# Kernel optimization log

Hardware: AMD Instinct MI355X
Metric: run time of the kernel (lower is better)

Reference implementation:

```python
import jax, jax.numpy as jnp
import numpy as np

ALPHA = 1.0
N, P, D = 8192, 128, 256
NUM_CLASSES = 128


def setup_inputs() -> dict:
    key = jax.random.key(0)
    kx, ky, kp = jax.random.split(key, 3)
    x = jax.random.normal(kx, (N, D), dtype=jnp.float32)
    y = jax.random.randint(ky, (N,), 0, NUM_CLASSES)
    prototypes = jax.random.normal(kp, (P, D), dtype=jnp.float32)
    return {"x": x, "y": y, "prototypes": prototypes}


def reference(x, y, prototypes):
    # (same math as the broadcasted sum((x-p)**2), expressed as a GEMM)
    x_sq = jnp.sum(x * x, axis=1, keepdims=True)          # [N, 1]
    p_sq = jnp.sum(prototypes * prototypes, axis=1)       # [P]
    dist = x_sq - 2.0 * jnp.einsum('nd,pd->np', x, prototypes) + p_sq[None, :]  # [N, P]

    # Torch code sets correct_mask[arange(N), y] = True, i.e. the "correct"
    # prototype is the one whose INDEX equals the class label y.
    n_idx = jnp.arange(dist.shape[0])
    d1 = dist[n_idx, y]                                    # [N] distance to correct prototype
    incorrect = jnp.where(jax.nn.one_hot(y, dist.shape[1], dtype=jnp.bool_),
                          jnp.inf, dist)
    d2 = jnp.min(incorrect, axis=1)                        # [N] min over wrong prototypes

    mu = (d1 - d2) / (d1 + d2)
    return jnp.mean(jax.nn.sigmoid(-ALPHA * mu))
```

## Files before the change

kernel.cpp:

```cpp
#include <hip/hip_runtime.h>
#include <math.h>

#define N_ROWS  8192
#define DIM     256
#define NPROTO  128
#define ROWS_PB 16
#define NBLK    (N_ROWS / ROWS_PB)
#define PSTR    264

typedef float f32x4 __attribute__((ext_vector_type(4)));
typedef short s16x8 __attribute__((ext_vector_type(8)));

__device__ __forceinline__ unsigned short f2bf(float f) {
  unsigned int u = __float_as_uint(f);
  u += 0x7fffu + ((u >> 16) & 1u);
  return (unsigned short)(u >> 16);
}

__global__ __launch_bounds__(256, 2) void glvq_kernel(
    const float* __restrict__ x, const int* __restrict__ y,
    const float* __restrict__ proto, float* __restrict__ out) {
  __shared__ unsigned short pT[NPROTO * PSTR];
  __shared__ unsigned short xT[ROWS_PB * PSTR];
  __shared__ float psq[NPROTO];
  __shared__ float xsq[ROWS_PB];
  __shared__ int   ylds[ROWS_PB];
  __shared__ float red1[4 * ROWS_PB];
  __shared__ float red2[4 * ROWS_PB];

  const int t = threadIdx.x;
  const int r0 = blockIdx.x * ROWS_PB;

  {
    const float4* p4 = (const float4*)proto;
#pragma unroll
    for (int j = 0; j < 16; ++j) {
      int c = j * 256 + t;
      float4 a = p4[c * 2];
      float4 b = p4[c * 2 + 1];
      int p = c >> 5;
      int ci = c & 31;
      union { s16x8 v; unsigned short u[8]; } pk;
      pk.u[0] = f2bf(a.x); pk.u[1] = f2bf(a.y); pk.u[2] = f2bf(a.z); pk.u[3] = f2bf(a.w);
      pk.u[4] = f2bf(b.x); pk.u[5] = f2bf(b.y); pk.u[6] = f2bf(b.z); pk.u[7] = f2bf(b.w);
      *(s16x8*)&pT[p * PSTR + ci * 8] = pk.v;
      float s = a.x * a.x + a.y * a.y + a.z * a.z + a.w * a.w +
                b.x * b.x + b.y * b.y + b.z * b.z + b.w * b.w;
#pragma unroll
      for (int m = 1; m <= 16; m <<= 1) s += __shfl_xor(s, m);
      if ((t & 31) == 0) psq[j * 8 + (t >> 5)] = s;
    }
  }

  {
    const float4* x4 = (const float4*)x;
    int r = t >> 4, ci = t & 15;
    const float4* xr = x4 + (size_t)(r0 + r) * (DIM / 4);
    float s = 0.f;
#pragma unroll
    for (int j = 0; j < 4; ++j) {
      float4 v = xr[ci + 16 * j];
      s += v.x * v.x + v.y * v.y + v.z * v.z + v.w * v.w;
      uint2 w2;
      w2.x = (unsigned)f2bf(v.x) | ((unsigned)f2bf(v.y) << 16);
      w2.y = (unsigned)f2bf(v.z) | ((unsigned)f2bf(v.w) << 16);
      *(uint2*)&xT[r * PSTR + (ci + 16 * j) * 4] = w2;
    }
#pragma unroll
    for (int m = 1; m <= 8; m <<= 1) s += __shfl_xor(s, m);
    if (ci == 0) xsq[r] = s;
    if (t < ROWS_PB) ylds[t] = y[r0 + t];
  }
  __syncthreads();

  const int l = t & 63;
  const int w = t >> 6;
  const int mq = l >> 4;
  const int mc = l & 15;
  f32x4 acc0 = {0.f, 0.f, 0.f, 0.f};
  f32x4 acc1 = {0.f, 0.f, 0.f, 0.f};
  const unsigned short* aptr = &xT[mc * PSTR + mq * 8];
  const unsigned short* b0p  = &pT[(w * 32 + mc) * PSTR + mq * 8];
  const unsigned short* b1p  = b0p + 16 * PSTR;
#pragma unroll
  for (int ks = 0; ks < 8; ++ks) {
    s16x8 af  = *(const s16x8*)(aptr + ks * 32);
    s16x8 bf0 = *(const s16x8*)(b0p + ks * 32);
    s16x8 bf1 = *(const s16x8*)(b1p + ks * 32);
    acc0 = __builtin_amdgcn_mfma_f32_16x16x32_bf16(af, bf0, acc0, 0, 0, 0);
    acc1 = __builtin_amdgcn_mfma_f32_16x16x32_bf16(af, bf1, acc1, 0, 0, 0);
  }

  const int p0i = w * 32 + mc;
  const int p1i = p0i + 16;
  const float pq0 = psq[p0i];
  const float pq1 = psq[p1i];
  float r1[4], r2[4];
#pragma unroll
  for (int reg = 0; reg < 4; ++reg) {
    int m = mq * 4 + reg;
    float xs = xsq[m];
    int ym = ylds[m];
    float d0 = xs + pq0 - 2.f * acc0[reg];
    float d1_ = xs + pq1 - 2.f * acc1[reg];
    float dd1 = 1e30f, dd2 = 1e30f;
    if (p0i == ym) dd1 = d0; else dd2 = d0;
    if (p1i == ym) dd1 = fminf(dd1, d1_); else dd2 = fminf(dd2, d1_);
    r1[reg] = dd1;
    r2[reg] = dd2;
  }
#pragma unroll
  for (int m = 1; m <= 8; m <<= 1) {
#pragma unroll
    for (int reg = 0; reg < 4; ++reg) {
      r1[reg] = fminf(r1[reg], __shfl_xor(r1[reg], m));
      r2[reg] = fminf(r2[reg], __shfl_xor(r2[reg], m));
    }
  }
  if (mc == 0) {
#pragma unroll
    for (int reg = 0; reg < 4; ++reg) {
      red1[w * ROWS_PB + mq * 4 + reg] = r1[reg];
      red2[w * ROWS_PB + mq * 4 + reg] = r2[reg];
    }
  }
  __syncthreads();

  if (t < ROWS_PB) {
    float d1 = 1e30f, d2 = 1e30f;
#pragma unroll
    for (int wv = 0; wv < 4; ++wv) {
      d1 = fminf(d1, red1[wv * ROWS_PB + t]);
      d2 = fminf(d2, red2[wv * ROWS_PB + t]);
    }
    float mu = (d1 - d2) / (d1 + d2);
    float s = 1.f / (1.f + __expf(mu));
#pragma unroll
    for (int m = 1; m <= 8; m <<= 1) s += __shfl_xor(s, m);
    if (t == 0) atomicAdd(out, s * (1.f / (float)N_ROWS));
  }
}

extern "C" void kernel_launch(void* const* d_in, const int* in_sizes, int n_in,
                              void* d_out, int out_size, void* d_ws, size_t ws_size,
                              hipStream_t stream) {
  const float* x = (const float*)d_in[0];
  const int* y = (const int*)d_in[1];
  const float* proto = (const float*)d_in[2];
  float* out = (float*)d_out;

  hipMemsetAsync(out, 0, sizeof(float), stream);
  glvq_kernel<<<NBLK, 256, 0, stream>>>(x, y, proto, out);
}
```

Before: 75.94 us.

## Precompute bf16 prototypes and norms in a prep kernel shared by all blocks

Adds a small prep kernel that converts the prototypes to bf16 once, computes their squared norms and zeroes the output, replacing the memset. The main kernel then loads the prebuilt bf16 prototypes straight into LDS, halving the per-block prototype read and removing the per-block conversion and shuffle reductions. The cost is an extra kernel launch with a dependency on it, plus workspace traffic.

```diff
diff --git a/kernel.cpp b/kernel.cpp
--- a/kernel.cpp
+++ b/kernel.cpp
@@ -17,9 +17,26 @@
   return (unsigned short)(u >> 16);
 }
 
+__global__ __launch_bounds__(256) void glvq_prep_kernel(
+    const float* __restrict__ proto, unsigned short* __restrict__ pbf,
+    float* __restrict__ psq, float* __restrict__ out) {
+  const int tid = blockIdx.x * 256 + threadIdx.x;
+  float4 v = ((const float4*)proto)[tid];
+  uint2 w2;
+  w2.x = (unsigned)f2bf(v.x) | ((unsigned)f2bf(v.y) << 16);
+  w2.y = (unsigned)f2bf(v.z) | ((unsigned)f2bf(v.w) << 16);
+  *(uint2*)&pbf[tid * 4] = w2;
+  float s = v.x * v.x + v.y * v.y + v.z * v.z + v.w * v.w;
+#pragma unroll
+  for (int m = 1; m <= 32; m <<= 1) s += __shfl_xor(s, m);
+  if ((threadIdx.x & 63) == 0) psq[tid >> 6] = s;
+  if (tid == 0) out[0] = 0.f;
+}
+
 __global__ __launch_bounds__(256, 2) void glvq_kernel(
     const float* __restrict__ x, const int* __restrict__ y,
-    const float* __restrict__ proto, float* __restrict__ out) {
+    const unsigned short* __restrict__ pbf, const float* __restrict__ psq_g,
+    float* __restrict__ out) {
   __shared__ unsigned short pT[NPROTO * PSTR];
   __shared__ unsigned short xT[ROWS_PB * PSTR];
   __shared__ float psq[NPROTO];
@@ -32,24 +49,16 @@
   const int r0 = blockIdx.x * ROWS_PB;
 
   {
-    const float4* p4 = (const float4*)proto;
+    const uint4* src = (const uint4*)pbf;
 #pragma unroll
     for (int j = 0; j < 16; ++j) {
       int c = j * 256 + t;
-      float4 a = p4[c * 2];
-      float4 b = p4[c * 2 + 1];
+      uint4 v = src[c];
       int p = c >> 5;
       int ci = c & 31;
-      union { s16x8 v; unsigned short u[8]; } pk;
-      pk.u[0] = f2bf(a.x); pk.u[1] = f2bf(a.y); pk.u[2] = f2bf(a.z); pk.u[3] = f2bf(a.w);
-      pk.u[4] = f2bf(b.x); pk.u[5] = f2bf(b.y); pk.u[6] = f2bf(b.z); pk.u[7] = f2bf(b.w);
-      *(s16x8*)&pT[p * PSTR + ci * 8] = pk.v;
-      float s = a.x * a.x + a.y * a.y + a.z * a.z + a.w * a.w +
-                b.x * b.x + b.y * b.y + b.z * b.z + b.w * b.w;
-#pragma unroll
-      for (int m = 1; m <= 16; m <<= 1) s += __shfl_xor(s, m);
-      if ((t & 31) == 0) psq[j * 8 + (t >> 5)] = s;
+      *(uint4*)&pT[p * PSTR + ci * 8] = v;
     }
+    if (t < NPROTO) psq[t] = psq_g[t];
   }
 
   {
@@ -149,6 +158,9 @@
   const float* proto = (const float*)d_in[2];
   float* out = (float*)d_out;
 
-  hipMemsetAsync(out, 0, sizeof(float), stream);
-  glvq_kernel<<<NBLK, 256, 0, stream>>>(x, y, proto, out);
+  unsigned short* pbf = (unsigned short*)d_ws;
+  float* psq = (float*)((char*)d_ws + NPROTO * DIM * 2);
+
+  glvq_prep_kernel<<<32, 256, 0, stream>>>(proto, pbf, psq, out);
+  glvq_kernel<<<NBLK, 256, 0, stream>>>(x, y, pbf, psq, out);
 }
```

After: 70.78 us. 1.07x faster.

## Precompute bf16 prototypes in prep kernel, async-load to LDS with XOR swizzle

Applied to the files above, without the earlier changes.

Adds a small prep kernel that converts prototypes to bf16 once, computes their squared norms and zeroes the output, replacing the memset. The main kernel then copies the pre-swizzled bf16 prototypes straight into LDS with global_load_lds, so each of the 512 blocks no longer redoes the fp32 load and conversion. LDS padding is replaced by an XOR swizzle on both the x and prototype tiles, which is meant to avoid bank conflicts while shrinking LDS use. The cost is an extra kernel launch and a dependency on the workspace buffer.

```diff
diff --git a/kernel.cpp b/kernel.cpp
--- a/kernel.cpp
+++ b/kernel.cpp
@@ -6,7 +6,6 @@
 #define NPROTO  128
 #define ROWS_PB 16
 #define NBLK    (N_ROWS / ROWS_PB)
-#define PSTR    264
 
 typedef float f32x4 __attribute__((ext_vector_type(4)));
 typedef short s16x8 __attribute__((ext_vector_type(8)));
@@ -17,11 +16,40 @@
   return (unsigned short)(u >> 16);
 }
 
+__device__ __forceinline__ void gl_lds16(const void* g, void* l) {
+  __builtin_amdgcn_global_load_lds(
+      (const __attribute__((address_space(1))) void*)g,
+      (__attribute__((address_space(3))) void*)l, 16, 0, 0);
+}
+
+__global__ __launch_bounds__(256) void glvq_prep_kernel(
+    const float* __restrict__ proto, unsigned short* __restrict__ pbf,
+    float* __restrict__ psq, float* __restrict__ out) {
+  const int tid = blockIdx.x * 256 + threadIdx.x;
+  const int row = tid >> 5;
+  const int co  = tid & 31;
+  const float4* p4 = (const float4*)proto;
+  float4 a = p4[tid * 2];
+  float4 b = p4[tid * 2 + 1];
+  union { s16x8 v; unsigned short u[8]; } pk;
+  pk.u[0] = f2bf(a.x); pk.u[1] = f2bf(a.y); pk.u[2] = f2bf(a.z); pk.u[3] = f2bf(a.w);
+  pk.u[4] = f2bf(b.x); pk.u[5] = f2bf(b.y); pk.u[6] = f2bf(b.z); pk.u[7] = f2bf(b.w);
+  const int slot = row * 32 + (co ^ (row & 7));
+  *(s16x8*)&pbf[slot * 8] = pk.v;
+  float s = a.x * a.x + a.y * a.y + a.z * a.z + a.w * a.w +
+            b.x * b.x + b.y * b.y + b.z * b.z + b.w * b.w;
+#pragma unroll
+  for (int m = 1; m <= 16; m <<= 1) s += __shfl_xor(s, m);
+  if (co == 0) psq[row] = s;
+  if (tid == 0) out[0] = 0.f;
+}
+
 __global__ __launch_bounds__(256, 2) void glvq_kernel(
     const float* __restrict__ x, const int* __restrict__ y,
-    const float* __restrict__ proto, float* __restrict__ out) {
-  __shared__ unsigned short pT[NPROTO * PSTR];
-  __shared__ unsigned short xT[ROWS_PB * PSTR];
+    const unsigned short* __restrict__ pbf, const float* __restrict__ psq_g,
+    float* __restrict__ out) {
+  __shared__ unsigned short pT[NPROTO * 256];
+  __shared__ unsigned short xT[ROWS_PB * 256];
   __shared__ float psq[NPROTO];
   __shared__ float xsq[ROWS_PB];
   __shared__ int   ylds[ROWS_PB];
@@ -31,45 +59,33 @@
   const int t = threadIdx.x;
   const int r0 = blockIdx.x * ROWS_PB;
 
-  {
-    const float4* p4 = (const float4*)proto;
 #pragma unroll
-    for (int j = 0; j < 16; ++j) {
-      int c = j * 256 + t;
-      float4 a = p4[c * 2];
-      float4 b = p4[c * 2 + 1];
-      int p = c >> 5;
-      int ci = c & 31;
-      union { s16x8 v; unsigned short u[8]; } pk;
-      pk.u[0] = f2bf(a.x); pk.u[1] = f2bf(a.y); pk.u[2] = f2bf(a.z); pk.u[3] = f2bf(a.w);
-      pk.u[4] = f2bf(b.x); pk.u[5] = f2bf(b.y); pk.u[6] = f2bf(b.z); pk.u[7] = f2bf(b.w);
-      *(s16x8*)&pT[p * PSTR + ci * 8] = pk.v;
-      float s = a.x * a.x + a.y * a.y + a.z * a.z + a.w * a.w +
-                b.x * b.x + b.y * b.y + b.z * b.z + b.w * b.w;
-#pragma unroll
-      for (int m = 1; m <= 16; m <<= 1) s += __shfl_xor(s, m);
-      if ((t & 31) == 0) psq[j * 8 + (t >> 5)] = s;
-    }
+  for (int j = 0; j < 16; ++j) {
+    int c = j * 256 + t;
+    gl_lds16((const char*)pbf + (size_t)c * 16, (char*)pT + (size_t)c * 16);
   }
+  if (t < NPROTO) psq[t] = psq_g[t];
+  if (t < ROWS_PB) ylds[t] = y[r0 + t];
 
   {
-    const float4* x4 = (const float4*)x;
-    int r = t >> 4, ci = t & 15;
-    const float4* xr = x4 + (size_t)(r0 + r) * (DIM / 4);
-    float s = 0.f;
-#pragma unroll
-    for (int j = 0; j < 4; ++j) {
-      float4 v = xr[ci + 16 * j];
-      s += v.x * v.x + v.y * v.y + v.z * v.z + v.w * v.w;
-      uint2 w2;
-      w2.x = (unsigned)f2bf(v.x) | ((unsigned)f2bf(v.y) << 16);
-      w2.y = (unsigned)f2bf(v.z) | ((unsigned)f2bf(v.w) << 16);
-      *(uint2*)&xT[r * PSTR + (ci + 16 * j) * 4] = w2;
-    }
+    const int r = t >> 4, i = t & 15;
+    const float4* xr = (const float4*)x + (size_t)(r0 + r) * 64 + i * 4;
+    float4 v0 = xr[0], v1 = xr[1], v2 = xr[2], v3 = xr[3];
+    union { s16x8 v; unsigned short u[8]; } pk0, pk1;
+    pk0.u[0] = f2bf(v0.x); pk0.u[1] = f2bf(v0.y); pk0.u[2] = f2bf(v0.z); pk0.u[3] = f2bf(v0.w);
+    pk0.u[4] = f2bf(v1.x); pk0.u[5] = f2bf(v1.y); pk0.u[6] = f2bf(v1.z); pk0.u[7] = f2bf(v1.w);
+    pk1.u[0] = f2bf(v2.x); pk1.u[1] = f2bf(v2.y); pk1.u[2] = f2bf(v2.z); pk1.u[3] = f2bf(v2.w);
+    pk1.u[4] = f2bf(v3.x); pk1.u[5] = f2bf(v3.y); pk1.u[6] = f2bf(v3.z); pk1.u[7] = f2bf(v3.w);
+    const int r7 = r & 7;
+    *(s16x8*)&xT[(r * 32 + ((2 * i) ^ r7)) * 8] = pk0.v;
+    *(s16x8*)&xT[(r * 32 + ((2 * i + 1) ^ r7)) * 8] = pk1.v;
+    float s = v0.x * v0.x + v0.y * v0.y + v0.z * v0.z + v0.w * v0.w +
+              v1.x * v1.x + v1.y * v1.y + v1.z * v1.z + v1.w * v1.w +
+              v2.x * v2.x + v2.y * v2.y + v2.z * v2.z + v2.w * v2.w +
+              v3.x * v3.x + v3.y * v3.y + v3.z * v3.z + v3.w * v3.w;
 #pragma unroll
     for (int m = 1; m <= 8; m <<= 1) s += __shfl_xor(s, m);
-    if (ci == 0) xsq[r] = s;
-    if (t < ROWS_PB) ylds[t] = y[r0 + t];
+    if (i == 0) xsq[r] = s;
   }
   __syncthreads();
 
@@ -77,16 +93,18 @@
   const int w = t >> 6;
   const int mq = l >> 4;
   const int mc = l & 15;
+  const int m7 = mc & 7;
   f32x4 acc0 = {0.f, 0.f, 0.f, 0.f};
   f32x4 acc1 = {0.f, 0.f, 0.f, 0.f};
-  const unsigned short* aptr = &xT[mc * PSTR + mq * 8];
-  const unsigned short* b0p  = &pT[(w * 32 + mc) * PSTR + mq * 8];
-  const unsigned short* b1p  = b0p + 16 * PSTR;
+  const unsigned short* xbase = &xT[mc * 256];
+  const unsigned short* b0p = &pT[(w * 32 + mc) * 256];
+  const unsigned short* b1p = b0p + 16 * 256;
 #pragma unroll
   for (int ks = 0; ks < 8; ++ks) {
-    s16x8 af  = *(const s16x8*)(aptr + ks * 32);
-    s16x8 bf0 = *(const s16x8*)(b0p + ks * 32);
-    s16x8 bf1 = *(const s16x8*)(b1p + ks * 32);
+    const int off = ((mq + 4 * ks) ^ m7) * 8;
+    s16x8 af  = *(const s16x8*)(xbase + off);
+    s16x8 bf0 = *(const s16x8*)(b0p + off);
+    s16x8 bf1 = *(const s16x8*)(b1p + off);
     acc0 = __builtin_amdgcn_mfma_f32_16x16x32_bf16(af, bf0, acc0, 0, 0, 0);
     acc1 = __builtin_amdgcn_mfma_f32_16x16x32_bf16(af, bf1, acc1, 0, 0, 0);
   }
@@ -149,6 +167,9 @@
   const float* proto = (const float*)d_in[2];
   float* out = (float*)d_out;
 
-  hipMemsetAsync(out, 0, sizeof(float), stream);
-  glvq_kernel<<<NBLK, 256, 0, stream>>>(x, y, proto, out);
+  unsigned short* pbf = (unsigned short*)d_ws;
+  float* psq = (float*)((char*)d_ws + NPROTO * DIM * 2);
+
+  glvq_prep_kernel<<<16, 256, 0, stream>>>(proto, pbf, psq, out);
+  glvq_kernel<<<NBLK, 256, 0, stream>>>(x, y, pbf, psq, out);
 }
```

Result: faster. 71.06 us (-6.4%).
